# Optimization experiments

Hardware: AMD Instinct MI355X
Metric: run time of the kernel (lower is better)

Reference implementation:

```python
import jax, jax.numpy as jnp
import numpy as np

B, S, H, D = 4, 2048, 12, 64
HIDDEN = H * D  # 768
WINDOW = 64     # config.local_attention // 2
ROPE_THETA = 10000.0  # local_rope_theta for sliding layers


def rotate_half(x):
    d = x.shape[-1] // 2
    return jnp.concatenate([-x[..., d:], x[..., :d]], axis=-1)


def setup_inputs() -> dict:
    key = jax.random.key(0)
    k1, k2, k3 = jax.random.split(key, 3)
    hidden_states = jax.random.normal(k1, (B, S, HIDDEN), dtype=jnp.float32)
    # RoPE tables (HF style): inv_freq over half dims, duplicated
    inv_freq = 1.0 / (ROPE_THETA ** (jnp.arange(0, D, 2, dtype=jnp.float32) / D))  # [D/2]
    pos = jnp.arange(S, dtype=jnp.float32)
    freqs = pos[:, None] * inv_freq[None, :]          # [S, D/2]
    emb = jnp.concatenate([freqs, freqs], axis=-1)    # [S, D]
    cos = jnp.broadcast_to(jnp.cos(emb)[None], (B, S, D))
    sin = jnp.broadcast_to(jnp.sin(emb)[None], (B, S, D))
    # sliding-window additive mask [B,1,S,S]
    idx = jnp.arange(S)
    allowed = jnp.abs(idx[:, None] - idx[None, :]) <= WINDOW
    neg = jnp.finfo(jnp.float32).min
    attention_mask = jnp.broadcast_to(
        jnp.where(allowed, 0.0, neg)[None, None], (B, 1, S, S)
    ).astype(jnp.float32)
    std = 0.02
    Wqkv_w = jax.random.normal(k2, (3 * HIDDEN, HIDDEN), dtype=jnp.float32) * std
    Wo_w = jax.random.normal(k3, (HIDDEN, HIDDEN), dtype=jnp.float32) * std
    return {"hidden_states": hidden_states, "cos": cos, "sin": sin,
            "attention_mask": attention_mask, "Wqkv_w": Wqkv_w, "Wo_w": Wo_w}


def reference(hidden_states, cos, sin, attention_mask, Wqkv_w, Wo_w):
    b, s, _ = hidden_states.shape
    scaling = D ** -0.5
    qkv = hidden_states @ Wqkv_w.T                       # [B,S,3*HIDDEN]
    qkv = qkv.reshape(b, s, 3, H, D)
    q = jnp.transpose(qkv[:, :, 0], (0, 2, 1, 3))        # [B,H,S,D]
    k = jnp.transpose(qkv[:, :, 1], (0, 2, 1, 3))
    v = jnp.transpose(qkv[:, :, 2], (0, 2, 1, 3))
    # RoPE with float32 intermediates (inputs already fp32 here)
    c = cos[:, None].astype(jnp.float32)                 # [B,1,S,D]
    sn = sin[:, None].astype(jnp.float32)
    qf, kf = q.astype(jnp.float32), k.astype(jnp.float32)
    q = (qf * c + rotate_half(qf) * sn).astype(q.dtype)
    k = (kf * c + rotate_half(kf) * sn).astype(k.dtype)
    # SDPA with explicit additive mask
    scores = jnp.einsum('bhqd,bhkd->bhqk', q, k) * scaling + attention_mask
    attn = jax.nn.softmax(scores, axis=-1)
    out = jnp.einsum('bhqk,bhkd->bhqd', attn, v)         # [B,H,S,D]
    out = jnp.transpose(out, (0, 2, 1, 3)).reshape(b, s, HIDDEN)
    return out @ Wo_w.T
```

## Files before the change

kernel.cpp:

```cpp
#include <hip/hip_runtime.h>
#include <math.h>


typedef __attribute__((ext_vector_type(8))) short short8;
typedef __attribute__((ext_vector_type(4))) float floatx4;

constexpr int kB = 4;
constexpr int kS = 2048;
constexpr int kH = 12;
constexpr int kD = 64;
constexpr int kHidden = 768;
constexpr int kQKV = 3 * kHidden;

__device__ __forceinline__ unsigned short f2bf(float f) {
  union { float f; unsigned int u; } x; x.f = f;
  unsigned int r = (x.u + 0x7fffu + ((x.u >> 16) & 1u)) >> 16;
  return (unsigned short)r;
}

__global__ __launch_bounds__(256) void cvt_bf16(const float* __restrict__ in,
                                                unsigned short* __restrict__ out,
                                                int n4) {
  const int i = blockIdx.x * 256 + threadIdx.x;
  if (i >= n4) return;
  const float4 v = ((const float4*)in)[i];
  ushort4 o;
  o.x = f2bf(v.x); o.y = f2bf(v.y); o.z = f2bf(v.z); o.w = f2bf(v.w);
  ((ushort4*)out)[i] = o;
}

__device__ __forceinline__ void gload_lds16(const unsigned short* g, unsigned short* l) {
  __builtin_amdgcn_global_load_lds(
      (const __attribute__((address_space(1))) unsigned int*)g,
      (__attribute__((address_space(3))) unsigned int*)l, 16, 0, 0);
}

__global__ __launch_bounds__(256) void gemm_qkv(
    const unsigned short* __restrict__ A,
    const unsigned short* __restrict__ B,
    const float* __restrict__ cosp, const float* __restrict__ sinp,
    unsigned short* __restrict__ Qr, unsigned short* __restrict__ Kr,
    unsigned short* __restrict__ Vt) {
  constexpr int K = kHidden;
  __shared__ unsigned short As[128 * 64];
  __shared__ unsigned short Bs[128 * 64];

  const int tid = threadIdx.x;
  const int lane = tid & 63;
  const int wave = tid >> 6;
  const int m0 = blockIdx.x * 128;
  const int n0 = blockIdx.y * 128;

  int ldsS[4];
  const unsigned short* gA[4];
  const unsigned short* gB[4];
#pragma unroll
  for (int t = 0; t < 4; t++) {
    const int ci = (wave * 4 + t) * 64 + lane;
    const int row = ci >> 3;
    const int c = (ci & 7) ^ (row & 7);
    ldsS[t] = ci * 8;
    gA[t] = A + (size_t)(m0 + row) * K + c * 8;
    gB[t] = B + (size_t)(n0 + row) * K + c * 8;
  }

  const int wm = wave >> 1, wn = wave & 1;
  const int mr = wm * 64 + (lane & 15);
  const int nr = wn * 64 + (lane & 15);
  const int kq = lane >> 4;

  floatx4 acc[4][4];
#pragma unroll
  for (int i = 0; i < 4; i++)
#pragma unroll
    for (int j = 0; j < 4; j++) acc[i][j] = (floatx4)(0.f);

  for (int k0 = 0; k0 < K; k0 += 64) {
    if (k0) __syncthreads();
#pragma unroll
    for (int t = 0; t < 4; t++) {
      gload_lds16(gA[t] + k0, &As[ldsS[t]]);
      gload_lds16(gB[t] + k0, &Bs[ldsS[t]]);
    }
    __syncthreads();
#pragma unroll
    for (int s = 0; s < 2; s++) {
      short8 af[4], bf[4];
#pragma unroll
      for (int i = 0; i < 4; i++) {
        af[i] = *(const short8*)&As[(mr + i * 16) * 64 + (((s * 4 + kq) ^ (mr & 7)) * 8)];
        bf[i] = *(const short8*)&Bs[(nr + i * 16) * 64 + (((s * 4 + kq) ^ (nr & 7)) * 8)];
      }
#pragma unroll
      for (int i = 0; i < 4; i++)
#pragma unroll
        for (int j = 0; j < 4; j++)
          acc[i][j] = __builtin_amdgcn_mfma_f32_16x16x32_bf16(af[i], bf[j],
                                                              acc[i][j], 0, 0, 0);
    }
  }

  const int region = n0 / kHidden;
  const int crow = m0 + wm * 64 + kq * 4;
  const int ccol0 = (n0 % kHidden) + wn * 64 + (lane & 15);

  if (region == 2) {
#pragma unroll
    for (int i = 0; i < 4; i++)
#pragma unroll
      for (int r = 0; r < 4; r++) {
        const int m = crow + i * 16 + r;
        const int b = m >> 11, s = m & 2047;
#pragma unroll
        for (int j = 0; j < 4; j++) {
          const int cr = ccol0 + j * 16;
          const int h = cr >> 6, d = cr & 63;
          Vt[((size_t)(b * kH + h) * kD + d) * kS + s] = f2bf(acc[i][j][r]);
        }
      }
  } else {
    unsigned short* dst = (region == 0) ? Qr : Kr;
    const float qscale = (region == 0) ? 0.125f : 1.f;
#pragma unroll
    for (int i = 0; i < 4; i++)
#pragma unroll
      for (int r = 0; r < 4; r++) {
        const int m = crow + i * 16 + r;
        const int b = m >> 11, s = m & 2047;
        const float* cs = cosp + ((size_t)(b * kS + s)) * kD;
        const float* sns = sinp + ((size_t)(b * kS + s)) * kD;
#pragma unroll
        for (int jp = 0; jp < 2; jp++) {
          const int cr = ccol0 + jp * 16;
          const int h = cr >> 6, d = cr & 63;
          const float c = cs[d], sn = sns[d];
          const float xlo = acc[i][jp][r], xhi = acc[i][jp + 2][r];
          unsigned short* o = dst + (((size_t)(b * kH + h)) * kS + s) * kD + d;
          o[0]  = f2bf((xlo * c - xhi * sn) * qscale);
          o[32] = f2bf((xhi * c + xlo * sn) * qscale);
        }
      }
  }
}

__global__ __launch_bounds__(256) void gemm_bf16_nt(
    const unsigned short* __restrict__ A, const unsigned short* __restrict__ B,
    float* __restrict__ C, int M, int N, int K) {
  __shared__ unsigned short As[128 * 64];
  __shared__ unsigned short Bs[128 * 64];

  const int tid = threadIdx.x;
  const int lane = tid & 63;
  const int wave = tid >> 6;
  const int m0 = blockIdx.x * 128;
  const int n0 = blockIdx.y * 128;

  int ldsS[4];
  const unsigned short* gA[4];
  const unsigned short* gB[4];
#pragma unroll
  for (int t = 0; t < 4; t++) {
    const int ci = (wave * 4 + t) * 64 + lane;
    const int row = ci >> 3;
    const int c = (ci & 7) ^ (row & 7);
    ldsS[t] = ci * 8;
    gA[t] = A + (size_t)(m0 + row) * K + c * 8;
    gB[t] = B + (size_t)(n0 + row) * K + c * 8;
  }

  const int wm = wave >> 1, wn = wave & 1;
  const int mr = wm * 64 + (lane & 15);
  const int nr = wn * 64 + (lane & 15);
  const int kq = lane >> 4;

  floatx4 acc[4][4];
#pragma unroll
  for (int i = 0; i < 4; i++)
#pragma unroll
    for (int j = 0; j < 4; j++) acc[i][j] = (floatx4)(0.f);

  for (int k0 = 0; k0 < K; k0 += 64) {
    if (k0) __syncthreads();
#pragma unroll
    for (int t = 0; t < 4; t++) {
      gload_lds16(gA[t] + k0, &As[ldsS[t]]);
      gload_lds16(gB[t] + k0, &Bs[ldsS[t]]);
    }
    __syncthreads();
#pragma unroll
    for (int s = 0; s < 2; s++) {
      short8 af[4], bf[4];
#pragma unroll
      for (int i = 0; i < 4; i++) {
        af[i] = *(const short8*)&As[(mr + i * 16) * 64 + (((s * 4 + kq) ^ (mr & 7)) * 8)];
        bf[i] = *(const short8*)&Bs[(nr + i * 16) * 64 + (((s * 4 + kq) ^ (nr & 7)) * 8)];
      }
#pragma unroll
      for (int i = 0; i < 4; i++)
#pragma unroll
        for (int j = 0; j < 4; j++)
          acc[i][j] = __builtin_amdgcn_mfma_f32_16x16x32_bf16(af[i], bf[j],
                                                              acc[i][j], 0, 0, 0);
    }
  }

  const int crow = m0 + wm * 64 + kq * 4;
  const int ccol = n0 + wn * 64 + (lane & 15);
#pragma unroll
  for (int i = 0; i < 4; i++)
#pragma unroll
    for (int r = 0; r < 4; r++) {
      float* cp = C + (size_t)(crow + i * 16 + r) * N + ccol;
#pragma unroll
      for (int j = 0; j < 4; j++) cp[j * 16] = acc[i][j][r];
    }
}

constexpr int AQT = 32;

__global__ __launch_bounds__(256) void attn_v3(
    const unsigned short* __restrict__ Qr, const unsigned short* __restrict__ Kr,
    const unsigned short* __restrict__ Vt, unsigned short* __restrict__ out) {
  __shared__ unsigned short Pfrag[2][5][64][8];
  __shared__ float Mx[2][AQT];
  __shared__ float Ssum[2][AQT];

  const int tid = threadIdx.x;
  const int lane = tid & 63;
  const int wave = tid >> 6;
  const int quad = lane >> 4;
  const int l15 = lane & 15;
  const int qbase = blockIdx.x * AQT;
  const int h = blockIdx.y, b = blockIdx.z;
  const int bh = b * kH + h;
  const int kbase = qbase - 64;
  const int tq = wave >> 1;
  const int kh = wave & 1;

  short8 vf[2][5];
  {
    const unsigned short* vbase = Vt + (size_t)bh * kD * kS;
#pragma unroll
    for (int nt = 0; nt < 2; nt++) {
      const unsigned short* vrow = vbase + (size_t)(kh * 32 + nt * 16 + l15) * kS;
#pragma unroll
      for (int kk = 0; kk < 5; kk++) {
        int s0 = kbase + kk * 32 + quad * 8;
        s0 = min(max(s0, 0), kS - 8);
        vf[nt][kk] = *(const short8*)(vrow + s0);
      }
    }
  }

  const unsigned short* qsrc =
      Qr + ((size_t)bh * kS + qbase + tq * 16 + l15) * kD + quad * 8;
  const short8 a0 = *(const short8*)qsrc;
  const short8 a1 = *(const short8*)(qsrc + 32);

  floatx4 acc[5];
  const unsigned short* ksrc = Kr + (size_t)bh * kS * kD;
#pragma unroll
  for (int g = 0; g < 5; g++) {
    int row = kbase + (kh * 5 + g) * 16 + l15;
    row = min(max(row, 0), kS - 1);
    const unsigned short* kp = ksrc + (size_t)row * kD + quad * 8;
    const short8 b0 = *(const short8*)kp;
    const short8 b1 = *(const short8*)(kp + 32);
    floatx4 z = (floatx4)(0.f);
    z = __builtin_amdgcn_mfma_f32_16x16x32_bf16(a0, b0, z, 0, 0, 0);
    z = __builtin_amdgcn_mfma_f32_16x16x32_bf16(a1, b1, z, 0, 0, 0);
    acc[g] = z;
  }

  float mx4[4];
#pragma unroll
  for (int r = 0; r < 4; r++) {
    const int q = tq * 16 + quad * 4 + r;
    float m = -3.0e38f;
#pragma unroll
    for (int g = 0; g < 5; g++) {
      const int key = (kh * 5 + g) * 16 + l15;
      const int kg_ = kbase + key;
      const bool valid = (key >= q) && (key <= q + 128) && (kg_ >= 0) && (kg_ < kS);
      const float sc = valid ? acc[g][r] : -3.0e38f;
      acc[g][r] = sc;
      m = fmaxf(m, sc);
    }
#pragma unroll
    for (int off = 1; off < 16; off <<= 1) m = fmaxf(m, __shfl_xor(m, off, 64));
    mx4[r] = m;
  }
  if (l15 == 0) {
#pragma unroll
    for (int r = 0; r < 4; r++) Mx[kh][tq * 16 + quad * 4 + r] = mx4[r];
  }
  __syncthreads();

#pragma unroll
  for (int r = 0; r < 4; r++) {
    const int q = tq * 16 + quad * 4 + r;
    const float m = fmaxf(mx4[r], Mx[kh ^ 1][q]);
    float s = 0.f;
#pragma unroll
    for (int g = 0; g < 5; g++) {
      const int key = (kh * 5 + g) * 16 + l15;
      const float e = (acc[g][r] > -1.0e38f) ? __expf(acc[g][r] - m) : 0.f;
      s += e;
      Pfrag[tq][key >> 5][((key >> 3) & 3) * 16 + quad * 4 + r][key & 7] = f2bf(e);
    }
#pragma unroll
    for (int off = 1; off < 16; off <<= 1) s += __shfl_xor(s, off, 64);
    if (l15 == 0) Ssum[kh][q] = s;
  }
  __syncthreads();

  floatx4 o0 = (floatx4)(0.f), o1 = (floatx4)(0.f);
#pragma unroll
  for (int kk = 0; kk < 5; kk++) {
    const short8 pa = *(const short8*)&Pfrag[tq][kk][lane][0];
    o0 = __builtin_amdgcn_mfma_f32_16x16x32_bf16(pa, vf[0][kk], o0, 0, 0, 0);
    o1 = __builtin_amdgcn_mfma_f32_16x16x32_bf16(pa, vf[1][kk], o1, 0, 0, 0);
  }

#pragma unroll
  for (int r = 0; r < 4; r++) {
    const int q = tq * 16 + quad * 4 + r;
    const float inv = 1.f / (Ssum[0][q] + Ssum[1][q]);
    unsigned short* op =
        out + ((size_t)(b * kS + qbase + q)) * kHidden + h * kD + kh * 32 + l15;
    op[0] = f2bf(o0[r] * inv);
    op[16] = f2bf(o1[r] * inv);
  }
}

extern "C" void kernel_launch(void* const* d_in, const int* in_sizes, int n_in,
                              void* d_out, int out_size, void* d_ws,
                              size_t ws_size, hipStream_t stream) {
  const float* hidden = (const float*)d_in[0];
  const float* cosp = (const float*)d_in[1];
  const float* sinp = (const float*)d_in[2];
  const float* wqkv = (const float*)d_in[4];
  const float* wo = (const float*)d_in[5];
  float* out = (float*)d_out;

  const int M = kB * kS;
  const size_t szH = (size_t)M * kHidden;

  unsigned short* hbf = (unsigned short*)d_ws;
  unsigned short* wqkvbf = hbf + szH;
  unsigned short* wobf = wqkvbf + (size_t)kQKV * kHidden;
  unsigned short* attnbf = wobf + (size_t)kHidden * kHidden;
  unsigned short* Qrb = attnbf + szH;
  unsigned short* Krb = Qrb + szH;
  unsigned short* Vtb = Krb + szH;

  cvt_bf16<<<(M * kHidden / 4) / 256, 256, 0, stream>>>(hidden, hbf,
                                                        M * kHidden / 4);
  cvt_bf16<<<(kQKV * kHidden / 4) / 256, 256, 0, stream>>>(
      wqkv, wqkvbf, kQKV * kHidden / 4);
  cvt_bf16<<<(kHidden * kHidden / 4) / 256, 256, 0, stream>>>(
      wo, wobf, kHidden * kHidden / 4);

  dim3 g1(M / 128, kQKV / 128);
  gemm_qkv<<<g1, 256, 0, stream>>>(hbf, wqkvbf, cosp, sinp, Qrb, Krb, Vtb);

  dim3 ga(kS / AQT, kH, kB);
  attn_v3<<<ga, 256, 0, stream>>>(Qrb, Krb, Vtb, attnbf);

  dim3 g2(M / 128, kHidden / 128);
  gemm_bf16_nt<<<g2, 256, 0, stream>>>(attnbf, wobf, out, M, kHidden, kHidden);
}
```

Before: 227.8 us.

## Fuse conversion launches, stage QKV epilogue through LDS, drop softmax max pass

```diff
diff --git a/kernel.cpp b/kernel.cpp
--- a/kernel.cpp
+++ b/kernel.cpp
@@ -18,15 +18,27 @@
   return (unsigned short)r;
 }
 
-__global__ __launch_bounds__(256) void cvt_bf16(const float* __restrict__ in,
-                                                unsigned short* __restrict__ out,
-                                                int n4) {
-  const int i = blockIdx.x * 256 + threadIdx.x;
-  if (i >= n4) return;
-  const float4 v = ((const float4*)in)[i];
+__global__ __launch_bounds__(256) void cvt_all(
+    const float* __restrict__ h, const float* __restrict__ wqkv,
+    const float* __restrict__ wo, unsigned short* __restrict__ hb,
+    unsigned short* __restrict__ wqb, unsigned short* __restrict__ wob) {
+  constexpr int n1 = kB * kS * kHidden / 4;
+  constexpr int n2 = kQKV * kHidden / 4;
+  constexpr int n3 = kHidden * kHidden / 4;
+  int i = blockIdx.x * 256 + threadIdx.x;
+  const float* src;
+  unsigned short* dst;
+  if (i < n1) {
+    src = h; dst = hb;
+  } else if (i < n1 + n2) {
+    i -= n1; src = wqkv; dst = wqb;
+  } else {
+    i -= n1 + n2; if (i >= n3) return; src = wo; dst = wob;
+  }
+  const float4 v = ((const float4*)src)[i];
   ushort4 o;
   o.x = f2bf(v.x); o.y = f2bf(v.y); o.z = f2bf(v.z); o.w = f2bf(v.w);
-  ((ushort4*)out)[i] = o;
+  ((ushort4*)dst)[i] = o;
 }
 
 __device__ __forceinline__ void gload_lds16(const unsigned short* g, unsigned short* l) {
@@ -42,8 +54,9 @@
     unsigned short* __restrict__ Qr, unsigned short* __restrict__ Kr,
     unsigned short* __restrict__ Vt) {
   constexpr int K = kHidden;
-  __shared__ unsigned short As[128 * 64];
-  __shared__ unsigned short Bs[128 * 64];
+  __shared__ unsigned short SH[128 * 136];
+  unsigned short* As = SH;
+  unsigned short* Bs = SH + 128 * 64;
 
   const int tid = threadIdx.x;
   const int lane = tid & 63;
@@ -100,24 +113,33 @@
     }
   }
 
+  __syncthreads();
+  unsigned short (*Obuf)[136] = (unsigned short (*)[136])SH;
+
   const int region = n0 / kHidden;
-  const int crow = m0 + wm * 64 + kq * 4;
-  const int ccol0 = (n0 % kHidden) + wn * 64 + (lane & 15);
+  const int b = m0 >> 11, s0 = m0 & 2047;
+  const int h0 = (n0 % kHidden) >> 6;
+  const int rowL0 = wm * 64 + kq * 4;
 
   if (region == 2) {
 #pragma unroll
     for (int i = 0; i < 4; i++)
 #pragma unroll
       for (int r = 0; r < 4; r++) {
-        const int m = crow + i * 16 + r;
-        const int b = m >> 11, s = m & 2047;
-#pragma unroll
-        for (int j = 0; j < 4; j++) {
-          const int cr = ccol0 + j * 16;
-          const int h = cr >> 6, d = cr & 63;
-          Vt[((size_t)(b * kH + h) * kD + d) * kS + s] = f2bf(acc[i][j][r]);
-        }
-      }
+        const int rowL = rowL0 + i * 16 + r;
+#pragma unroll
+        for (int j = 0; j < 4; j++)
+          Obuf[wn * 64 + j * 16 + (lane & 15)][rowL] = f2bf(acc[i][j][r]);
+      }
+    __syncthreads();
+#pragma unroll
+    for (int it = 0; it < 8; it++) {
+      const int t = tid + it * 256;
+      const int s8 = t & 15, rowc = t >> 4;
+      const int hl = rowc >> 6, d = rowc & 63;
+      *(short8*)(Vt + ((size_t)(b * kH + h0 + hl) * kD + d) * kS + s0 + s8 * 8) =
+          *(const short8*)&Obuf[rowc][s8 * 8];
+    }
   } else {
     unsigned short* dst = (region == 0) ? Qr : Kr;
     const float qscale = (region == 0) ? 0.125f : 1.f;
@@ -125,21 +147,28 @@
     for (int i = 0; i < 4; i++)
 #pragma unroll
       for (int r = 0; r < 4; r++) {
-        const int m = crow + i * 16 + r;
-        const int b = m >> 11, s = m & 2047;
+        const int rowL = rowL0 + i * 16 + r;
+        const int s = s0 + rowL;
         const float* cs = cosp + ((size_t)(b * kS + s)) * kD;
         const float* sns = sinp + ((size_t)(b * kS + s)) * kD;
 #pragma unroll
         for (int jp = 0; jp < 2; jp++) {
-          const int cr = ccol0 + jp * 16;
-          const int h = cr >> 6, d = cr & 63;
+          const int colL = wn * 64 + jp * 16 + (lane & 15);
+          const int d = colL & 63;
           const float c = cs[d], sn = sns[d];
           const float xlo = acc[i][jp][r], xhi = acc[i][jp + 2][r];
-          unsigned short* o = dst + (((size_t)(b * kH + h)) * kS + s) * kD + d;
-          o[0]  = f2bf((xlo * c - xhi * sn) * qscale);
-          o[32] = f2bf((xhi * c + xlo * sn) * qscale);
+          Obuf[rowL][colL]      = f2bf((xlo * c - xhi * sn) * qscale);
+          Obuf[rowL][colL + 32] = f2bf((xhi * c + xlo * sn) * qscale);
         }
       }
+    __syncthreads();
+#pragma unroll
+    for (int it = 0; it < 8; it++) {
+      const int t = tid + it * 256;
+      const int d8 = t & 7, sl = (t >> 3) & 127, hl = t >> 10;
+      *(short8*)(dst + ((size_t)(b * kH + h0 + hl) * kS + s0 + sl) * kD + d8 * 8) =
+          *(const short8*)&Obuf[sl][hl * 64 + d8 * 8];
+    }
   }
 }
 
@@ -222,7 +251,6 @@
     const unsigned short* __restrict__ Qr, const unsigned short* __restrict__ Kr,
     const unsigned short* __restrict__ Vt, unsigned short* __restrict__ out) {
   __shared__ unsigned short Pfrag[2][5][64][8];
-  __shared__ float Mx[2][AQT];
   __shared__ float Ssum[2][AQT];
 
   const int tid = threadIdx.x;
@@ -272,39 +300,16 @@
     acc[g] = z;
   }
 
-  float mx4[4];
 #pragma unroll
   for (int r = 0; r < 4; r++) {
     const int q = tq * 16 + quad * 4 + r;
-    float m = -3.0e38f;
+    float s = 0.f;
 #pragma unroll
     for (int g = 0; g < 5; g++) {
       const int key = (kh * 5 + g) * 16 + l15;
       const int kg_ = kbase + key;
       const bool valid = (key >= q) && (key <= q + 128) && (kg_ >= 0) && (kg_ < kS);
-      const float sc = valid ? acc[g][r] : -3.0e38f;
-      acc[g][r] = sc;
-      m = fmaxf(m, sc);
-    }
-#pragma unroll
-    for (int off = 1; off < 16; off <<= 1) m = fmaxf(m, __shfl_xor(m, off, 64));
-    mx4[r] = m;
-  }
-  if (l15 == 0) {
-#pragma unroll
-    for (int r = 0; r < 4; r++) Mx[kh][tq * 16 + quad * 4 + r] = mx4[r];
-  }
-  __syncthreads();
-
-#pragma unroll
-  for (int r = 0; r < 4; r++) {
-    const int q = tq * 16 + quad * 4 + r;
-    const float m = fmaxf(mx4[r], Mx[kh ^ 1][q]);
-    float s = 0.f;
-#pragma unroll
-    for (int g = 0; g < 5; g++) {
-      const int key = (kh * 5 + g) * 16 + l15;
-      const float e = (acc[g][r] > -1.0e38f) ? __expf(acc[g][r] - m) : 0.f;
+      const float e = valid ? __expf(acc[g][r]) : 0.f;
       s += e;
       Pfrag[tq][key >> 5][((key >> 3) & 3) * 16 + quad * 4 + r][key & 7] = f2bf(e);
     }
@@ -354,12 +359,9 @@
   unsigned short* Krb = Qrb + szH;
   unsigned short* Vtb = Krb + szH;
 
-  cvt_bf16<<<(M * kHidden / 4) / 256, 256, 0, stream>>>(hidden, hbf,
-                                                        M * kHidden / 4);
-  cvt_bf16<<<(kQKV * kHidden / 4) / 256, 256, 0, stream>>>(
-      wqkv, wqkvbf, kQKV * kHidden / 4);
-  cvt_bf16<<<(kHidden * kHidden / 4) / 256, 256, 0, stream>>>(
-      wo, wobf, kHidden * kHidden / 4);
+  const int ncvt = (M * kHidden + kQKV * kHidden + kHidden * kHidden) / 4;
+  cvt_all<<<(ncvt + 255) / 256, 256, 0, stream>>>(hidden, wqkv, wo, hbf,
+                                                  wqkvbf, wobf);
 
   dim3 g1(M / 128, kQKV / 128);
   gemm_qkv<<<g1, 256, 0, stream>>>(hbf, wqkvbf, cosp, sinp, Qrb, Krb, Vtb);
```

Result: faster. 210.9 us (-7.4%).
